# Kernel optimization log

Hardware: AMD Instinct MI355X
Metric: run time of the kernel (lower is better)

Reference implementation:

```python
import jax, jax.numpy as jnp
import numpy as np

N_NODES = 50000
N_EDGES = 800000
IN_DIM = 256
HIDDEN = 32
HEADS = 4
OUT_DIM = 64


def setup_inputs() -> dict:
    key = jax.random.key(0)
    k1, k2, k3, k4, k5, k6, k7 = jax.random.split(key, 7)
    h = jax.random.normal(k1, (N_NODES, IN_DIM), dtype=jnp.float32)
    src = jax.random.randint(k2, (N_EDGES,), 0, N_NODES, dtype=jnp.int32)
    dst = jax.random.randint(k3, (N_EDGES,), 0, N_NODES, dtype=jnp.int32)
    # xavier_normal with relu gain, per-head weights
    gain = float(np.sqrt(2.0))
    W1 = gain * jnp.sqrt(2.0 / (IN_DIM + HIDDEN)) * jax.random.normal(k4, (HEADS, IN_DIM, HIDDEN), dtype=jnp.float32)
    a1 = gain * jnp.sqrt(2.0 / (2 * HIDDEN + 1)) * jax.random.normal(k5, (HEADS, 2 * HIDDEN), dtype=jnp.float32)
    W2 = gain * jnp.sqrt(2.0 / (HIDDEN * HEADS + OUT_DIM)) * jax.random.normal(k6, (1, HIDDEN * HEADS, OUT_DIM), dtype=jnp.float32)
    a2 = gain * jnp.sqrt(2.0 / (2 * OUT_DIM + 1)) * jax.random.normal(k7, (1, 2 * OUT_DIM), dtype=jnp.float32)
    return {"h": h, "src": src, "dst": dst, "W1": W1, "a1": a1, "W2": W2, "a2": a2}


def _gat_layer(x, src, dst, W, a):
    # x: [N, in], W: [H, in, d], a: [H, 2d]
    N = x.shape[0]
    d = W.shape[-1]
    z = jnp.einsum('ni,hio->nho', x, W)                    # [N, H, d]
    a_s, a_d = a[:, :d], a[:, d:]
    es = jnp.einsum('nho,ho->nh', z, a_s)                  # per-node src score
    ed = jnp.einsum('nho,ho->nh', z, a_d)                  # per-node dst score
    e = jax.nn.leaky_relu(es[src] + ed[dst])               # [E, H]
    # segment (per-destination) softmax over incoming edges
    emax = jax.ops.segment_max(e, dst, num_segments=N)     # [N, H]
    ex = jnp.exp(e - emax[dst])
    denom = jax.ops.segment_sum(ex, dst, num_segments=N)   # [N, H]
    alpha = ex / denom[dst]                                # [E, H]
    # scatter weighted sum of source feats back to destinations
    out = jax.ops.segment_sum(alpha[:, :, None] * z[src], dst, num_segments=N)  # [N, H, d]
    return out.reshape(N, -1)


def reference(h, src, dst, W1, a1, W2, a2):
    h1 = jax.nn.elu(_gat_layer(h, src, dst, W1, a1))       # [N, HEADS*HIDDEN]
    return _gat_layer(h1, src, dst, W2, a2)                # [N, OUT_DIM]
```

## Files before the change

### kernel.cpp

```cpp
#include <hip/hip_runtime.h>
#include <hip/hip_bf16.h>
#include <math.h>

#define N_NODES 50000
#define N_EDGES 800000
#define IN_DIM 256
#define HID 32
#define HEADS 4
#define OUT_DIM 64

#define SCAN_CHUNK 1024
#define SCAN_BLOCKS ((N_NODES + SCAN_CHUNK - 1) / SCAN_CHUNK)
#define HIST_BLOCKS ((N_EDGES + 255) / 256)
#define MBLK ((N_NODES + 63) / 64)

typedef __attribute__((ext_vector_type(8))) short bf16x8;
typedef __attribute__((ext_vector_type(4))) float f32x4;

__device__ __forceinline__ float lrelu(float e) { return e > 0.f ? e : 0.01f * e; }
__device__ __forceinline__ float bflo(unsigned u) { return __uint_as_float(u << 16); }
__device__ __forceinline__ float bfhi(unsigned u) { return __uint_as_float(u & 0xffff0000u); }

__device__ __forceinline__ unsigned short rne_bf16(float x) {
    unsigned u = __float_as_uint(x);
    unsigned r = u + 0x7fffu + ((u >> 16) & 1u);
    return (unsigned short)(r >> 16);
}

__device__ __forceinline__ void splitf(float x, short& hi, short& lo) {
    unsigned u = __float_as_uint(x);
    unsigned short h = (unsigned short)(u >> 16);
    float hf = __uint_as_float(((unsigned)h) << 16);
    float l = x - hf;
    unsigned short lb = (unsigned short)(__float_as_uint(l) >> 16);
    hi = (short)h;
    lo = (short)lb;
}


__device__ __forceinline__ void prep_body(int k, int c,
        const float* __restrict__ W1, const float* __restrict__ a1,
        const float* __restrict__ W2, const float* __restrict__ a2,
        unsigned short* __restrict__ B1h, unsigned short* __restrict__ B1l,
        unsigned short* __restrict__ B2h, unsigned short* __restrict__ B2l) {
    if (c < 144) {
        float val = 0.f;
        if (c < 128) {
            val = W1[(size_t)(c >> 5) * IN_DIM * HID + (size_t)k * HID + (c & 31)];
        } else if (c < 136) {
            int j = c - 128;
            int hd = (j < 4) ? j : (j - 4);
            int off = (j < 4) ? 0 : HID;
            const float* Wp = W1 + (size_t)hd * IN_DIM * HID + (size_t)k * HID;
            const float* ap = a1 + hd * 2 * HID + off;
            float s = 0.f;
            for (int o = 0; o < HID; o++) s += Wp[o] * ap[o];
            val = s;
        }
        unsigned short hi = rne_bf16(val);
        float hf = __uint_as_float(((unsigned)hi) << 16);
        unsigned short lo = rne_bf16(val - hf);
        int s_ = k >> 5, q = (k >> 3) & 3, j8 = k & 7;
        int nt = c >> 4, L = q * 16 + (c & 15);
        size_t idx = (((size_t)s_ * 9 + nt) * 64 + L) * 8 + j8;
        B1h[idx] = hi;
        B1l[idx] = lo;
    } else if (c >= 160 && c < 240 && k < 128) {
        int c2 = c - 160;
        float val = 0.f;
        if (c2 < 64) {
            val = W2[(size_t)k * OUT_DIM + c2];
        } else if (c2 < 66) {
            const float* ap = a2 + (c2 - 64) * OUT_DIM;
            const float* Wp = W2 + (size_t)k * OUT_DIM;
            float s = 0.f;
            for (int o = 0; o < OUT_DIM; o++) s += Wp[o] * ap[o];
            val = s;
        }
        unsigned short hi = rne_bf16(val);
        float hf = __uint_as_float(((unsigned)hi) << 16);
        unsigned short lo = rne_bf16(val - hf);
        int s_ = k >> 5, q = (k >> 3) & 3, j8 = k & 7;
        int nt = c2 >> 4, L = q * 16 + (c2 & 15);
        size_t idx = (((size_t)s_ * 5 + nt) * 64 + L) * 8 + j8;
        B2h[idx] = hi;
        B2l[idx] = lo;
    }
}


__global__ void __launch_bounds__(256) prep_hist_kernel(
        const float* __restrict__ W1, const float* __restrict__ a1,
        const float* __restrict__ W2, const float* __restrict__ a2,
        unsigned short* __restrict__ B1h, unsigned short* __restrict__ B1l,
        unsigned short* __restrict__ B2h, unsigned short* __restrict__ B2l,
        const int* __restrict__ dst, int* __restrict__ count,
        int* __restrict__ rank) {
    int bid = blockIdx.x;
    if (bid < 256) {
        prep_body(bid, threadIdx.x, W1, a1, W2, a2, B1h, B1l, B2h, B2l);
    } else {
        int i = (bid - 256) * 256 + threadIdx.x;
        if (i < N_EDGES) rank[i] = atomicAdd(&count[dst[i]], 1);
    }
}


__device__ __forceinline__ void scan1_body(int bid, int t, const int* __restrict__ count,
        int* __restrict__ rs_local, int* __restrict__ bs_prefix, int* sdata) {
    int base = bid * SCAN_CHUNK + t * 4;
    int v[4];
    int s = 0;
#pragma unroll
    for (int j = 0; j < 4; j++) {
        int idx = base + j;
        int x = (idx < N_NODES) ? count[idx] : 0;
        v[j] = x;
        s += x;
    }
    sdata[t] = s;
    __syncthreads();
    for (int off = 1; off < 256; off <<= 1) {
        int u = (t >= off) ? sdata[t - off] : 0;
        __syncthreads();
        sdata[t] += u;
        __syncthreads();
    }
    int excl = sdata[t] - s;
#pragma unroll
    for (int j = 0; j < 4; j++) {
        int idx = base + j;
        if (idx < N_NODES) rs_local[idx] = excl;
        excl += v[j];
    }
    if (t > bid && t < SCAN_BLOCKS) atomicAdd(&bs_prefix[t], sdata[255]);
}


__device__ __forceinline__ void proj1_body(int n0, int L,
        const float* __restrict__ h, const unsigned short* __restrict__ Bh,
        const unsigned short* __restrict__ Bl, __hip_bfloat16* __restrict__ z1b,
        float* __restrict__ es1, float* __restrict__ ed1) {
    int q = L >> 4, L15 = L & 15;
    int rowA = n0 + L15;
    int rrA = rowA < N_NODES ? rowA : N_NODES - 1;
    const float* hrow = h + (size_t)rrA * IN_DIM + q * 8;

    f32x4 acc[9];
#pragma unroll
    for (int nt = 0; nt < 9; nt++) acc[nt] = (f32x4)(0.f);

    float4 x0 = *(const float4*)(hrow);
    float4 x1 = *(const float4*)(hrow + 4);

#pragma unroll
    for (int s = 0; s < 8; s++) {
        int sn = (s < 7) ? s + 1 : 7;
        float4 p0 = *(const float4*)(hrow + sn * 32);
        float4 p1 = *(const float4*)(hrow + sn * 32 + 4);

        float xs[8] = {x0.x, x0.y, x0.z, x0.w, x1.x, x1.y, x1.z, x1.w};
        bf16x8 ah, al;
#pragma unroll
        for (int j = 0; j < 8; j++) {
            short hi, lo;
            splitf(xs[j], hi, lo);
            ah[j] = hi;
            al[j] = lo;
        }

        const bf16x8* bhp = (const bf16x8*)(Bh + ((size_t)s * 9 * 64) * 8 + (size_t)L * 8);
        const bf16x8* blp = (const bf16x8*)(Bl + ((size_t)s * 9 * 64) * 8 + (size_t)L * 8);
#pragma unroll
        for (int nt = 0; nt < 9; nt++) {
            bf16x8 bh = bhp[nt * 64];
            acc[nt] = __builtin_amdgcn_mfma_f32_16x16x32_bf16(ah, bh, acc[nt], 0, 0, 0);
            acc[nt] = __builtin_amdgcn_mfma_f32_16x16x32_bf16(al, bh, acc[nt], 0, 0, 0);
        }
        {
            bf16x8 bl8 = blp[8 * 64];
            acc[8] = __builtin_amdgcn_mfma_f32_16x16x32_bf16(ah, bl8, acc[8], 0, 0, 0);
        }
        x0 = p0;
        x1 = p1;
    }

#pragma unroll
    for (int r = 0; r < 4; r++) {
        int rowc = n0 + q * 4 + r;
        if (rowc < N_NODES) {
#pragma unroll
            for (int nt = 0; nt < 8; nt++)
                z1b[(size_t)rowc * 128 + nt * 16 + L15] = __float2bfloat16(acc[nt][r]);
            if (L15 < 4) es1[rowc * HEADS + L15] = acc[8][r];
            else if (L15 < 8) ed1[rowc * HEADS + (L15 - 4)] = acc[8][r];
        }
    }
}


__global__ void __launch_bounds__(256) scan_proj1_kernel(
        const float* __restrict__ h, const unsigned short* __restrict__ Bh,
        const unsigned short* __restrict__ Bl, __hip_bfloat16* __restrict__ z1b,
        float* __restrict__ es1, float* __restrict__ ed1,
        const int* __restrict__ count, int* __restrict__ rs_local,
        int* __restrict__ bs_prefix) {
    if (blockIdx.x < SCAN_BLOCKS) {
        __shared__ int sdata[256];
        scan1_body(blockIdx.x, threadIdx.x, count, rs_local, bs_prefix, sdata);
        return;
    }
    int wave = threadIdx.x >> 6;
    int L = threadIdx.x & 63;
    int n0 = (blockIdx.x - SCAN_BLOCKS) * 64 + wave * 16;
    proj1_body(n0, L, h, Bh, Bl, z1b, es1, ed1);
}


__global__ void scatter_kernel(const int* __restrict__ src, const int* __restrict__ dst,
                               const int* __restrict__ rank, const int* __restrict__ rs_local,
                               const int* __restrict__ bs_prefix, int* __restrict__ esrc) {
    int i = blockIdx.x * blockDim.x + threadIdx.x;
    if (i < N_EDGES) {
        int d = dst[i];
        esrc[rs_local[d] + bs_prefix[d >> 10] + rank[i]] = src[i];
    }
}


__global__ void __launch_bounds__(256) agg1_kernel(
        const __hip_bfloat16* __restrict__ z1b, const float* __restrict__ es1,
        const float* __restrict__ ed1, const int* __restrict__ rs_local,
        const int* __restrict__ bs_prefix, const int* __restrict__ count,
        const int* __restrict__ esrc, __hip_bfloat16* __restrict__ h1b) {
    int v = blockIdx.x * 4 + (threadIdx.x >> 6);
    int L = threadIdx.x & 63;
    int sub = L >> 4;
    int c16 = L & 15;
    int hd = c16 >> 2;
    int beg = rs_local[v] + bs_prefix[v >> 10], deg = count[v];
    float edv = ed1[v * HEADS + hd];
    const int* ep = esrc + beg;
    float lacc = 0.f;
    float acc[8];
#pragma unroll
    for (int i = 0; i < 8; i++) acc[i] = 0.f;
    const uint4* zq = (const uint4*)z1b;

    for (int j0 = 0; j0 < deg; j0 += 32) {
        int se[8];
        uint4 u[8];
        float ev[8];
#pragma unroll
        for (int g = 0; g < 8; g++) {
            if (j0 + g * 4 < deg) {
                int e = j0 + g * 4 + sub;
                se[g] = ep[(e < deg) ? e : 0];
            }
        }
#pragma unroll
        for (int g = 0; g < 8; g++) {
            if (j0 + g * 4 < deg) {
                u[g] = zq[(size_t)se[g] * 16 + c16];
                ev[g] = es1[se[g] * HEADS + hd];
            }
        }
#pragma unroll
        for (int g = 0; g < 8; g++) {
            if (j0 + g * 4 < deg) {
                bool val = (j0 + g * 4 + sub) < deg;
                float q = val ? __expf(lrelu(ev[g] + edv)) : 0.f;
                lacc += q;
                acc[0] = fmaf(q, bflo(u[g].x), acc[0]);
                acc[1] = fmaf(q, bfhi(u[g].x), acc[1]);
                acc[2] = fmaf(q, bflo(u[g].y), acc[2]);
                acc[3] = fmaf(q, bfhi(u[g].y), acc[3]);
                acc[4] = fmaf(q, bflo(u[g].z), acc[4]);
                acc[5] = fmaf(q, bfhi(u[g].z), acc[5]);
                acc[6] = fmaf(q, bflo(u[g].w), acc[6]);
                acc[7] = fmaf(q, bfhi(u[g].w), acc[7]);
            }
        }
    }
    lacc += __shfl_xor(lacc, 1);
    lacc += __shfl_xor(lacc, 2);
    lacc += __shfl_xor(lacc, 16);
    lacc += __shfl_xor(lacc, 32);
    lacc *= 0.25f;
#pragma unroll
    for (int i = 0; i < 8; i++) {
        acc[i] += __shfl_xor(acc[i], 16);
        acc[i] += __shfl_xor(acc[i], 32);
    }
    if (L < 16) {
        float inv = (deg > 0) ? 1.f / lacc : 0.f;
        unsigned w[4];
#pragma unroll
        for (int i = 0; i < 4; i++) {
            float r0 = acc[2 * i] * inv;
            float r1 = acc[2 * i + 1] * inv;
            r0 = r0 > 0.f ? r0 : __expf(r0) - 1.f;
            r1 = r1 > 0.f ? r1 : __expf(r1) - 1.f;
            w[i] = (unsigned)rne_bf16(r0) | ((unsigned)rne_bf16(r1) << 16);
        }
        uint4* dstp = (uint4*)(h1b + (size_t)v * 128 + c16 * 8);
        *dstp = make_uint4(w[0], w[1], w[2], w[3]);
    }
}


__global__ void __launch_bounds__(256) proj2_mfma(
        const __hip_bfloat16* __restrict__ h1b, const unsigned short* __restrict__ Bh,
        const unsigned short* __restrict__ Bl, __hip_bfloat16* __restrict__ z2b,
        float* __restrict__ es2, float* __restrict__ ed2) {
    int tid = threadIdx.x;
    int wave = tid >> 6;
    int L = tid & 63;
    int q = L >> 4, L15 = L & 15;
    int n0 = blockIdx.x * 64 + wave * 16;

    int rowA = n0 + L15;
    int rrA = rowA < N_NODES ? rowA : N_NODES - 1;
    const bf16x8* hq = (const bf16x8*)(h1b + (size_t)rrA * 128);

    f32x4 acc[5];
#pragma unroll
    for (int nt = 0; nt < 5; nt++) acc[nt] = (f32x4)(0.f);

#pragma unroll
    for (int s = 0; s < 4; s++) {
        bf16x8 a = hq[s * 4 + q];
        const bf16x8* bhp = (const bf16x8*)(Bh + ((size_t)s * 5 * 64) * 8 + (size_t)L * 8);
        const bf16x8* blp = (const bf16x8*)(Bl + ((size_t)s * 5 * 64) * 8 + (size_t)L * 8);
#pragma unroll
        for (int nt = 0; nt < 5; nt++)
            acc[nt] = __builtin_amdgcn_mfma_f32_16x16x32_bf16(a, bhp[nt * 64], acc[nt], 0, 0, 0);
        acc[4] = __builtin_amdgcn_mfma_f32_16x16x32_bf16(a, blp[4 * 64], acc[4], 0, 0, 0);
    }

#pragma unroll
    for (int r = 0; r < 4; r++) {
        int rowc = n0 + q * 4 + r;
        if (rowc < N_NODES) {
#pragma unroll
            for (int nt = 0; nt < 4; nt++)
                z2b[(size_t)rowc * OUT_DIM + nt * 16 + L15] = __float2bfloat16(acc[nt][r]);
            if (L15 == 0) es2[rowc] = acc[4][r];
            else if (L15 == 1) ed2[rowc] = acc[4][r];
        }
    }
}


__global__ void __launch_bounds__(256) agg2_kernel(
        const __hip_bfloat16* __restrict__ z2b, const float* __restrict__ es2,
        const float* __restrict__ ed2, const int* __restrict__ rs_local,
        const int* __restrict__ bs_prefix, const int* __restrict__ count,
        const int* __restrict__ esrc, float* __restrict__ out) {
    int v = blockIdx.x * 4 + (threadIdx.x >> 6);
    int L = threadIdx.x & 63;
    int sub = L >> 3;
    int c8 = L & 7;
    int beg = rs_local[v] + bs_prefix[v >> 10], deg = count[v];
    float edv = ed2[v];
    const int* ep = esrc + beg;
    float lacc = 0.f;
    float acc[8];
#pragma unroll
    for (int i = 0; i < 8; i++) acc[i] = 0.f;
    const uint4* zq = (const uint4*)z2b;

    for (int j0 = 0; j0 < deg; j0 += 32) {
        int se[4];
        uint4 u[4];
        float ev[4];
#pragma unroll
        for (int g = 0; g < 4; g++) {
            if (j0 + g * 8 < deg) {
                int e = j0 + g * 8 + sub;
                se[g] = ep[(e < deg) ? e : 0];
            }
        }
#pragma unroll
        for (int g = 0; g < 4; g++) {
            if (j0 + g * 8 < deg) {
                u[g] = zq[(size_t)se[g] * 8 + c8];
                ev[g] = es2[se[g]];
            }
        }
#pragma unroll
        for (int g = 0; g < 4; g++) {
            if (j0 + g * 8 < deg) {
                bool val = (j0 + g * 8 + sub) < deg;
                float q = val ? __expf(lrelu(ev[g] + edv)) : 0.f;
                lacc += q;
                acc[0] = fmaf(q, bflo(u[g].x), acc[0]);
                acc[1] = fmaf(q, bfhi(u[g].x), acc[1]);
                acc[2] = fmaf(q, bflo(u[g].y), acc[2]);
                acc[3] = fmaf(q, bfhi(u[g].y), acc[3]);
                acc[4] = fmaf(q, bflo(u[g].z), acc[4]);
                acc[5] = fmaf(q, bfhi(u[g].z), acc[5]);
                acc[6] = fmaf(q, bflo(u[g].w), acc[6]);
                acc[7] = fmaf(q, bfhi(u[g].w), acc[7]);
            }
        }
    }
    lacc += __shfl_xor(lacc, 8);
    lacc += __shfl_xor(lacc, 16);
    lacc += __shfl_xor(lacc, 32);
#pragma unroll
    for (int i = 0; i < 8; i++) {
        acc[i] += __shfl_xor(acc[i], 8);
        acc[i] += __shfl_xor(acc[i], 16);
        acc[i] += __shfl_xor(acc[i], 32);
    }
    if (L < 8) {
        float inv = (deg > 0) ? 1.f / lacc : 0.f;
        float4 r0, r1;
#pragma unroll
        for (int i = 0; i < 8; i++) {
            float r = acc[i] * inv;
            if (i < 4) (&r0.x)[i] = r;
            else (&r1.x)[i - 4] = r;
        }
        float* dstp = out + (size_t)v * OUT_DIM + c8 * 8;
        *(float4*)dstp = r0;
        *(float4*)(dstp + 4) = r1;
    }
}


extern "C" void kernel_launch(void* const* d_in, const int* in_sizes, int n_in,
                              void* d_out, int out_size, void* d_ws, size_t ws_size,
                              hipStream_t stream) {
    const float* h  = (const float*)d_in[0];
    const int* src  = (const int*)d_in[1];
    const int* dst  = (const int*)d_in[2];
    const float* W1 = (const float*)d_in[3];
    const float* a1 = (const float*)d_in[4];
    const float* W2 = (const float*)d_in[5];
    const float* a2 = (const float*)d_in[6];
    float* out = (float*)d_out;

    char* w = (char*)d_ws;
    size_t off = 0;
    auto alloc = [&](size_t bytes) {
        void* p = w + off;
        off = (off + bytes + 255) & ~(size_t)255;
        return p;
    };
    __hip_bfloat16* z1b = (__hip_bfloat16*)alloc((size_t)N_NODES * 128 * 2);
    float* es1 = (float*)alloc((size_t)N_NODES * HEADS * 4);
    float* ed1 = (float*)alloc((size_t)N_NODES * HEADS * 4);
    __hip_bfloat16* h1b = (__hip_bfloat16*)alloc((size_t)N_NODES * 128 * 2);
    __hip_bfloat16* z2b = (__hip_bfloat16*)alloc((size_t)N_NODES * OUT_DIM * 2);
    float* es2 = (float*)alloc((size_t)N_NODES * 4);
    float* ed2 = (float*)alloc((size_t)N_NODES * 4);
    int* count     = (int*)alloc((size_t)(N_NODES + 64) * 4);
    int* bs_prefix = count + N_NODES;
    int* rs_local  = (int*)alloc((size_t)N_NODES * 4);
    int* rank      = (int*)alloc((size_t)N_EDGES * 4);
    int* esrc      = (int*)alloc((size_t)N_EDGES * 4);
    unsigned short* Bf1h = (unsigned short*)alloc((size_t)8 * 9 * 64 * 8 * 2);
    unsigned short* Bf1l = (unsigned short*)alloc((size_t)8 * 9 * 64 * 8 * 2);
    unsigned short* Bf2h = (unsigned short*)alloc((size_t)4 * 5 * 64 * 8 * 2);
    unsigned short* Bf2l = (unsigned short*)alloc((size_t)4 * 5 * 64 * 8 * 2);

    hipMemsetAsync(count, 0, (size_t)(N_NODES + 64) * 4, stream);

    prep_hist_kernel<<<256 + HIST_BLOCKS, 256, 0, stream>>>(
        W1, a1, W2, a2, Bf1h, Bf1l, Bf2h, Bf2l, dst, count, rank);

    scan_proj1_kernel<<<SCAN_BLOCKS + MBLK, 256, 0, stream>>>(
        h, Bf1h, Bf1l, z1b, es1, ed1, count, rs_local, bs_prefix);

    scatter_kernel<<<HIST_BLOCKS, 256, 0, stream>>>(src, dst, rank, rs_local, bs_prefix, esrc);

    agg1_kernel<<<N_NODES / 4, 256, 0, stream>>>(z1b, es1, ed1, rs_local, bs_prefix, count, esrc, h1b);
    proj2_mfma<<<MBLK, 256, 0, stream>>>(h1b, Bf2h, Bf2l, z2b, es2, ed2);
    agg2_kernel<<<N_NODES / 4, 256, 0, stream>>>(z2b, es2, ed2, rs_local, bs_prefix, count, esrc, out);
}
```

Before: 225.9 us.

## Rebalance kernel partitions to co-schedule proj1 with histogram and agg1 with proj2

Moves the degree histogram into the same launch as the first 500 proj1 tiles, and moves the scan into the launch with the remaining proj1 tiles. Splits agg1 at a node boundary so the second half of aggregation shares a launch with the proj2 tiles for the first half, followed by a small proj2 tail kernel. The memset is replaced by zeroing count inside the prep kernel. The aim is to fill idle CUs and cut launch gaps by overlapping independent work, at the cost of one extra launch and careful dependency ordering across the split ranges.

```diff
diff --git a/kernel.cpp b/kernel.cpp
--- a/kernel.cpp
+++ b/kernel.cpp
@@ -13,6 +13,15 @@
 #define SCAN_BLOCKS ((N_NODES + SCAN_CHUNK - 1) / SCAN_CHUNK)
 #define HIST_BLOCKS ((N_EDGES + 255) / 256)
 #define MBLK ((N_NODES + 63) / 64)
+
+#define PS1 500
+#define PS2 (MBLK - PS1)
+
+#define AGG_SPLIT 25024
+#define AGG1A_BLKS (AGG_SPLIT / 4)
+#define AGG1B_BLKS ((N_NODES - AGG_SPLIT + 3) / 4)
+#define P2A_BLKS (AGG_SPLIT / 64)
+#define P2B_BLKS ((N_NODES - AGG_SPLIT + 63) / 64)
 
 typedef __attribute__((ext_vector_type(8))) short bf16x8;
 typedef __attribute__((ext_vector_type(4))) float f32x4;
@@ -89,51 +98,15 @@
 }
 
 
-__global__ void __launch_bounds__(256) prep_hist_kernel(
+__global__ void __launch_bounds__(256) prep_kernel(
         const float* __restrict__ W1, const float* __restrict__ a1,
         const float* __restrict__ W2, const float* __restrict__ a2,
         unsigned short* __restrict__ B1h, unsigned short* __restrict__ B1l,
         unsigned short* __restrict__ B2h, unsigned short* __restrict__ B2l,
-        const int* __restrict__ dst, int* __restrict__ count,
-        int* __restrict__ rank) {
-    int bid = blockIdx.x;
-    if (bid < 256) {
-        prep_body(bid, threadIdx.x, W1, a1, W2, a2, B1h, B1l, B2h, B2l);
-    } else {
-        int i = (bid - 256) * 256 + threadIdx.x;
-        if (i < N_EDGES) rank[i] = atomicAdd(&count[dst[i]], 1);
-    }
-}
-
-
-__device__ __forceinline__ void scan1_body(int bid, int t, const int* __restrict__ count,
-        int* __restrict__ rs_local, int* __restrict__ bs_prefix, int* sdata) {
-    int base = bid * SCAN_CHUNK + t * 4;
-    int v[4];
-    int s = 0;
-#pragma unroll
-    for (int j = 0; j < 4; j++) {
-        int idx = base + j;
-        int x = (idx < N_NODES) ? count[idx] : 0;
-        v[j] = x;
-        s += x;
-    }
-    sdata[t] = s;
-    __syncthreads();
-    for (int off = 1; off < 256; off <<= 1) {
-        int u = (t >= off) ? sdata[t - off] : 0;
-        __syncthreads();
-        sdata[t] += u;
-        __syncthreads();
-    }
-    int excl = sdata[t] - s;
-#pragma unroll
-    for (int j = 0; j < 4; j++) {
-        int idx = base + j;
-        if (idx < N_NODES) rs_local[idx] = excl;
-        excl += v[j];
-    }
-    if (t > bid && t < SCAN_BLOCKS) atomicAdd(&bs_prefix[t], sdata[255]);
+        int* __restrict__ count) {
+    int gid = blockIdx.x * 256 + threadIdx.x;
+    if (gid < N_NODES + 64) count[gid] = 0;
+    prep_body(blockIdx.x, threadIdx.x, W1, a1, W2, a2, B1h, B1l, B2h, B2l);
 }
 
 
@@ -199,7 +172,56 @@
 }
 
 
-__global__ void __launch_bounds__(256) scan_proj1_kernel(
+__global__ void __launch_bounds__(256) proj1_hist_kernel(
+        const float* __restrict__ h, const unsigned short* __restrict__ Bh,
+        const unsigned short* __restrict__ Bl, __hip_bfloat16* __restrict__ z1b,
+        float* __restrict__ es1, float* __restrict__ ed1,
+        const int* __restrict__ dst, int* __restrict__ count,
+        int* __restrict__ rank) {
+    int bid = blockIdx.x;
+    if (bid < PS1) {
+        int wave = threadIdx.x >> 6;
+        int L = threadIdx.x & 63;
+        proj1_body(bid * 64 + wave * 16, L, h, Bh, Bl, z1b, es1, ed1);
+    } else {
+        int i = (bid - PS1) * 256 + threadIdx.x;
+        if (i < N_EDGES) rank[i] = atomicAdd(&count[dst[i]], 1);
+    }
+}
+
+
+__device__ __forceinline__ void scan1_body(int bid, int t, const int* __restrict__ count,
+        int* __restrict__ rs_local, int* __restrict__ bs_prefix, int* sdata) {
+    int base = bid * SCAN_CHUNK + t * 4;
+    int v[4];
+    int s = 0;
+#pragma unroll
+    for (int j = 0; j < 4; j++) {
+        int idx = base + j;
+        int x = (idx < N_NODES) ? count[idx] : 0;
+        v[j] = x;
+        s += x;
+    }
+    sdata[t] = s;
+    __syncthreads();
+    for (int off = 1; off < 256; off <<= 1) {
+        int u = (t >= off) ? sdata[t - off] : 0;
+        __syncthreads();
+        sdata[t] += u;
+        __syncthreads();
+    }
+    int excl = sdata[t] - s;
+#pragma unroll
+    for (int j = 0; j < 4; j++) {
+        int idx = base + j;
+        if (idx < N_NODES) rs_local[idx] = excl;
+        excl += v[j];
+    }
+    if (t > bid && t < SCAN_BLOCKS) atomicAdd(&bs_prefix[t], sdata[255]);
+}
+
+
+__global__ void __launch_bounds__(256) scan_proj1b_kernel(
         const float* __restrict__ h, const unsigned short* __restrict__ Bh,
         const unsigned short* __restrict__ Bl, __hip_bfloat16* __restrict__ z1b,
         float* __restrict__ es1, float* __restrict__ ed1,
@@ -210,10 +232,10 @@
         scan1_body(blockIdx.x, threadIdx.x, count, rs_local, bs_prefix, sdata);
         return;
     }
+    int task = blockIdx.x - SCAN_BLOCKS + PS1;
     int wave = threadIdx.x >> 6;
     int L = threadIdx.x & 63;
-    int n0 = (blockIdx.x - SCAN_BLOCKS) * 64 + wave * 16;
-    proj1_body(n0, L, h, Bh, Bl, z1b, es1, ed1);
+    proj1_body(task * 64 + wave * 16, L, h, Bh, Bl, z1b, es1, ed1);
 }
 
 
@@ -228,13 +250,11 @@
 }
 
 
-__global__ void __launch_bounds__(256) agg1_kernel(
+__device__ __forceinline__ void agg1_body(int v, int L,
         const __hip_bfloat16* __restrict__ z1b, const float* __restrict__ es1,
         const float* __restrict__ ed1, const int* __restrict__ rs_local,
         const int* __restrict__ bs_prefix, const int* __restrict__ count,
         const int* __restrict__ esrc, __hip_bfloat16* __restrict__ h1b) {
-    int v = blockIdx.x * 4 + (threadIdx.x >> 6);
-    int L = threadIdx.x & 63;
     int sub = L >> 4;
     int c16 = L & 15;
     int hd = c16 >> 2;
@@ -309,16 +329,11 @@
 }
 
 
-__global__ void __launch_bounds__(256) proj2_mfma(
+__device__ __forceinline__ void proj2_body(int n0, int L,
         const __hip_bfloat16* __restrict__ h1b, const unsigned short* __restrict__ Bh,
         const unsigned short* __restrict__ Bl, __hip_bfloat16* __restrict__ z2b,
         float* __restrict__ es2, float* __restrict__ ed2) {
-    int tid = threadIdx.x;
-    int wave = tid >> 6;
-    int L = tid & 63;
     int q = L >> 4, L15 = L & 15;
-    int n0 = blockIdx.x * 64 + wave * 16;
-
     int rowA = n0 + L15;
     int rrA = rowA < N_NODES ? rowA : N_NODES - 1;
     const bf16x8* hq = (const bf16x8*)(h1b + (size_t)rrA * 128);
@@ -349,6 +364,46 @@
             else if (L15 == 1) ed2[rowc] = acc[4][r];
         }
     }
+}
+
+
+__global__ void __launch_bounds__(256) agg1a_kernel(
+        const __hip_bfloat16* __restrict__ z1b, const float* __restrict__ es1,
+        const float* __restrict__ ed1, const int* __restrict__ rs_local,
+        const int* __restrict__ bs_prefix, const int* __restrict__ count,
+        const int* __restrict__ esrc, __hip_bfloat16* __restrict__ h1b) {
+    int v = blockIdx.x * 4 + (threadIdx.x >> 6);
+    agg1_body(v, threadIdx.x & 63, z1b, es1, ed1, rs_local, bs_prefix, count, esrc, h1b);
+}
+
+
+__global__ void __launch_bounds__(256) agg1b_proj2a_kernel(
+        const __hip_bfloat16* __restrict__ z1b, const float* __restrict__ es1,
+        const float* __restrict__ ed1, const int* __restrict__ rs_local,
+        const int* __restrict__ bs_prefix, const int* __restrict__ count,
+        const int* __restrict__ esrc, __hip_bfloat16* __restrict__ h1b,
+        const unsigned short* __restrict__ B2h, const unsigned short* __restrict__ B2l,
+        __hip_bfloat16* __restrict__ z2b, float* __restrict__ es2,
+        float* __restrict__ ed2) {
+    int L = threadIdx.x & 63;
+    int wave = threadIdx.x >> 6;
+    if (blockIdx.x < AGG1B_BLKS) {
+        int v = AGG_SPLIT + blockIdx.x * 4 + wave;
+        agg1_body(v, L, z1b, es1, ed1, rs_local, bs_prefix, count, esrc, h1b);
+    } else {
+        int pb = blockIdx.x - AGG1B_BLKS;
+        proj2_body(pb * 64 + wave * 16, L, h1b, B2h, B2l, z2b, es2, ed2);
+    }
+}
+
+
+__global__ void __launch_bounds__(256) proj2b_kernel(
+        const __hip_bfloat16* __restrict__ h1b, const unsigned short* __restrict__ Bh,
+        const unsigned short* __restrict__ Bl, __hip_bfloat16* __restrict__ z2b,
+        float* __restrict__ es2, float* __restrict__ ed2) {
+    int wave = threadIdx.x >> 6;
+    int L = threadIdx.x & 63;
+    proj2_body(AGG_SPLIT + blockIdx.x * 64 + wave * 16, L, h1b, Bh, Bl, z2b, es2, ed2);
 }
 
 
@@ -466,17 +521,25 @@
     unsigned short* Bf2h = (unsigned short*)alloc((size_t)4 * 5 * 64 * 8 * 2);
     unsigned short* Bf2l = (unsigned short*)alloc((size_t)4 * 5 * 64 * 8 * 2);
 
-    hipMemsetAsync(count, 0, (size_t)(N_NODES + 64) * 4, stream);
-
-    prep_hist_kernel<<<256 + HIST_BLOCKS, 256, 0, stream>>>(
-        W1, a1, W2, a2, Bf1h, Bf1l, Bf2h, Bf2l, dst, count, rank);
-
-    scan_proj1_kernel<<<SCAN_BLOCKS + MBLK, 256, 0, stream>>>(
+    prep_kernel<<<256, 256, 0, stream>>>(W1, a1, W2, a2, Bf1h, Bf1l, Bf2h, Bf2l, count);
+
+    proj1_hist_kernel<<<PS1 + HIST_BLOCKS, 256, 0, stream>>>(
+        h, Bf1h, Bf1l, z1b, es1, ed1, dst, count, rank);
+
+    scan_proj1b_kernel<<<SCAN_BLOCKS + PS2, 256, 0, stream>>>(
         h, Bf1h, Bf1l, z1b, es1, ed1, count, rs_local, bs_prefix);
 
     scatter_kernel<<<HIST_BLOCKS, 256, 0, stream>>>(src, dst, rank, rs_local, bs_prefix, esrc);
 
-    agg1_kernel<<<N_NODES / 4, 256, 0, stream>>>(z1b, es1, ed1, rs_local, bs_prefix, count, esrc, h1b);
-    proj2_mfma<<<MBLK, 256, 0, stream>>>(h1b, Bf2h, Bf2l, z2b, es2, ed2);
-    agg2_kernel<<<N_NODES / 4, 256, 0, stream>>>(z2b, es2, ed2, rs_local, bs_prefix, count, esrc, out);
-}
+    agg1a_kernel<<<AGG1A_BLKS, 256, 0, stream>>>(
+        z1b, es1, ed1, rs_local, bs_prefix, count, esrc, h1b);
+
+    agg1b_proj2a_kernel<<<AGG1B_BLKS + P2A_BLKS, 256, 0, stream>>>(
+        z1b, es1, ed1, rs_local, bs_prefix, count, esrc, h1b,
+        Bf2h, Bf2l, z2b, es2, ed2);
+
+    proj2b_kernel<<<P2B_BLKS, 256, 0, stream>>>(h1b, Bf2h, Bf2l, z2b, es2, ed2);
+
+    agg2_kernel<<<N_NODES / 4, 256, 0, stream>>>(
+        z2b, es2, ed2, rs_local, bs_prefix, count, esrc, out);
+}
```

Measured after the change: 232.9 us. +3.1%, slower.

## Split layer-1 projection across scan and scatter launches; preload A operands

Applied to the files above, without the earlier changes.

The layer-1 projection blocks are split into two parts: the first part runs alongside the prefix-scan blocks and the rest runs alongside the edge-scatter blocks, replacing the separate scatter launch. This fills the otherwise short scatter kernel with MFMA work and balances the two launches. The projection and proj2 kernels also load all A-operand rows up front instead of software-prefetching them one step ahead, which raises register pressure. The split point is a fixed constant.

```diff
diff --git a/kernel.cpp b/kernel.cpp
--- a/kernel.cpp
+++ b/kernel.cpp
@@ -13,6 +13,9 @@
 #define SCAN_BLOCKS ((N_NODES + SCAN_CHUNK - 1) / SCAN_CHUNK)
 #define HIST_BLOCKS ((N_EDGES + 255) / 256)
 #define MBLK ((N_NODES + 63) / 64)
+
+#define PS1 500
+#define PS2 (MBLK - PS1)
 
 typedef __attribute__((ext_vector_type(8))) short bf16x8;
 typedef __attribute__((ext_vector_type(4))) float f32x4;
@@ -146,20 +149,21 @@
     int rrA = rowA < N_NODES ? rowA : N_NODES - 1;
     const float* hrow = h + (size_t)rrA * IN_DIM + q * 8;
 
+    float4 xv0[8], xv1[8];
+#pragma unroll
+    for (int s = 0; s < 8; s++) {
+        xv0[s] = *(const float4*)(hrow + s * 32);
+        xv1[s] = *(const float4*)(hrow + s * 32 + 4);
+    }
+
     f32x4 acc[9];
 #pragma unroll
     for (int nt = 0; nt < 9; nt++) acc[nt] = (f32x4)(0.f);
 
-    float4 x0 = *(const float4*)(hrow);
-    float4 x1 = *(const float4*)(hrow + 4);
-
 #pragma unroll
     for (int s = 0; s < 8; s++) {
-        int sn = (s < 7) ? s + 1 : 7;
-        float4 p0 = *(const float4*)(hrow + sn * 32);
-        float4 p1 = *(const float4*)(hrow + sn * 32 + 4);
-
-        float xs[8] = {x0.x, x0.y, x0.z, x0.w, x1.x, x1.y, x1.z, x1.w};
+        float xs[8] = {xv0[s].x, xv0[s].y, xv0[s].z, xv0[s].w,
+                       xv1[s].x, xv1[s].y, xv1[s].z, xv1[s].w};
         bf16x8 ah, al;
 #pragma unroll
         for (int j = 0; j < 8; j++) {
@@ -181,8 +185,6 @@
             bf16x8 bl8 = blp[8 * 64];
             acc[8] = __builtin_amdgcn_mfma_f32_16x16x32_bf16(ah, bl8, acc[8], 0, 0, 0);
         }
-        x0 = p0;
-        x1 = p1;
     }
 
 #pragma unroll
@@ -199,28 +201,37 @@
 }
 
 
-__global__ void __launch_bounds__(256) scan_proj1_kernel(
+__global__ void __launch_bounds__(256) proj1a_scan_kernel(
         const float* __restrict__ h, const unsigned short* __restrict__ Bh,
         const unsigned short* __restrict__ Bl, __hip_bfloat16* __restrict__ z1b,
         float* __restrict__ es1, float* __restrict__ ed1,
         const int* __restrict__ count, int* __restrict__ rs_local,
         int* __restrict__ bs_prefix) {
-    if (blockIdx.x < SCAN_BLOCKS) {
-        __shared__ int sdata[256];
-        scan1_body(blockIdx.x, threadIdx.x, count, rs_local, bs_prefix, sdata);
+    if (blockIdx.x < PS1) {
+        int wave = threadIdx.x >> 6;
+        int L = threadIdx.x & 63;
+        proj1_body(blockIdx.x * 64 + wave * 16, L, h, Bh, Bl, z1b, es1, ed1);
         return;
     }
-    int wave = threadIdx.x >> 6;
-    int L = threadIdx.x & 63;
-    int n0 = (blockIdx.x - SCAN_BLOCKS) * 64 + wave * 16;
-    proj1_body(n0, L, h, Bh, Bl, z1b, es1, ed1);
-}
-
-
-__global__ void scatter_kernel(const int* __restrict__ src, const int* __restrict__ dst,
-                               const int* __restrict__ rank, const int* __restrict__ rs_local,
-                               const int* __restrict__ bs_prefix, int* __restrict__ esrc) {
-    int i = blockIdx.x * blockDim.x + threadIdx.x;
+    __shared__ int sdata[256];
+    scan1_body(blockIdx.x - PS1, threadIdx.x, count, rs_local, bs_prefix, sdata);
+}
+
+
+__global__ void __launch_bounds__(256) proj1b_scatter_kernel(
+        const float* __restrict__ h, const unsigned short* __restrict__ Bh,
+        const unsigned short* __restrict__ Bl, __hip_bfloat16* __restrict__ z1b,
+        float* __restrict__ es1, float* __restrict__ ed1,
+        const int* __restrict__ src, const int* __restrict__ dst,
+        const int* __restrict__ rank, const int* __restrict__ rs_local,
+        const int* __restrict__ bs_prefix, int* __restrict__ esrc) {
+    if (blockIdx.x < PS2) {
+        int wave = threadIdx.x >> 6;
+        int L = threadIdx.x & 63;
+        proj1_body((blockIdx.x + PS1) * 64 + wave * 16, L, h, Bh, Bl, z1b, es1, ed1);
+        return;
+    }
+    int i = (blockIdx.x - PS2) * 256 + threadIdx.x;
     if (i < N_EDGES) {
         int d = dst[i];
         esrc[rs_local[d] + bs_prefix[d >> 10] + rank[i]] = src[i];
@@ -323,19 +334,22 @@
     int rrA = rowA < N_NODES ? rowA : N_NODES - 1;
     const bf16x8* hq = (const bf16x8*)(h1b + (size_t)rrA * 128);
 
+    bf16x8 av[4];
+#pragma unroll
+    for (int s = 0; s < 4; s++) av[s] = hq[s * 4 + q];
+
     f32x4 acc[5];
 #pragma unroll
     for (int nt = 0; nt < 5; nt++) acc[nt] = (f32x4)(0.f);
 
 #pragma unroll
     for (int s = 0; s < 4; s++) {
-        bf16x8 a = hq[s * 4 + q];
         const bf16x8* bhp = (const bf16x8*)(Bh + ((size_t)s * 5 * 64) * 8 + (size_t)L * 8);
         const bf16x8* blp = (const bf16x8*)(Bl + ((size_t)s * 5 * 64) * 8 + (size_t)L * 8);
 #pragma unroll
         for (int nt = 0; nt < 5; nt++)
-            acc[nt] = __builtin_amdgcn_mfma_f32_16x16x32_bf16(a, bhp[nt * 64], acc[nt], 0, 0, 0);
-        acc[4] = __builtin_amdgcn_mfma_f32_16x16x32_bf16(a, blp[4 * 64], acc[4], 0, 0, 0);
+            acc[nt] = __builtin_amdgcn_mfma_f32_16x16x32_bf16(av[s], bhp[nt * 64], acc[nt], 0, 0, 0);
+        acc[4] = __builtin_amdgcn_mfma_f32_16x16x32_bf16(av[s], blp[4 * 64], acc[4], 0, 0, 0);
     }
 
 #pragma unroll
@@ -471,12 +485,15 @@
     prep_hist_kernel<<<256 + HIST_BLOCKS, 256, 0, stream>>>(
         W1, a1, W2, a2, Bf1h, Bf1l, Bf2h, Bf2l, dst, count, rank);
 
-    scan_proj1_kernel<<<SCAN_BLOCKS + MBLK, 256, 0, stream>>>(
+    proj1a_scan_kernel<<<PS1 + SCAN_BLOCKS, 256, 0, stream>>>(
         h, Bf1h, Bf1l, z1b, es1, ed1, count, rs_local, bs_prefix);
 
-    scatter_kernel<<<HIST_BLOCKS, 256, 0, stream>>>(src, dst, rank, rs_local, bs_prefix, esrc);
-
-    agg1_kernel<<<N_NODES / 4, 256, 0, stream>>>(z1b, es1, ed1, rs_local, bs_prefix, count, esrc, h1b);
+    proj1b_scatter_kernel<<<PS2 + HIST_BLOCKS, 256, 0, stream>>>(
+        h, Bf1h, Bf1l, z1b, es1, ed1, src, dst, rank, rs_local, bs_prefix, esrc);
+
+    agg1_kernel<<<N_NODES / 4, 256, 0, stream>>>(
+        z1b, es1, ed1, rs_local, bs_prefix, count, esrc, h1b);
     proj2_mfma<<<MBLK, 256, 0, stream>>>(h1b, Bf2h, Bf2l, z2b, es2, ed2);
-    agg2_kernel<<<N_NODES / 4, 256, 0, stream>>>(z2b, es2, ed2, rs_local, bs_prefix, count, esrc, out);
-}
+    agg2_kernel<<<N_NODES / 4, 256, 0, stream>>>(
+        z2b, es2, ed2, rs_local, bs_prefix, count, esrc, out);
+}
```

Result: slower. 234.5 us (+3.8%).

## Replace per-edge rank array with cursor atomics and pack z1 stores in pairs

Applied to the files above, without the earlier changes.

The histogram pass no longer stores a per-edge rank. The scan initialises a per-node cursor, and the scatter kernel claims slots with an atomicAdd on that cursor, which removes the rank write and read traffic. The layer-1 projection now writes z1 as packed bf16 pairs. The W2 rows are permuted in prep to match the new column order of h1. proj2 also hoists its A-operand loads ahead of the MFMA loop. The cost is atomic contention in the scatter kernel and a non-deterministic edge order within each destination segment, which can change the summation order.

```diff
diff --git a/kernel.cpp b/kernel.cpp
--- a/kernel.cpp
+++ b/kernel.cpp
@@ -67,12 +67,13 @@
         B1l[idx] = lo;
     } else if (c >= 160 && c < 240 && k < 128) {
         int c2 = c - 160;
+        int ck = (2 * (k >> 5) + (k & 1)) * 16 + ((k & 31) >> 1);
         float val = 0.f;
         if (c2 < 64) {
-            val = W2[(size_t)k * OUT_DIM + c2];
+            val = W2[(size_t)ck * OUT_DIM + c2];
         } else if (c2 < 66) {
             const float* ap = a2 + (c2 - 64) * OUT_DIM;
-            const float* Wp = W2 + (size_t)k * OUT_DIM;
+            const float* Wp = W2 + (size_t)ck * OUT_DIM;
             float s = 0.f;
             for (int o = 0; o < OUT_DIM; o++) s += Wp[o] * ap[o];
             val = s;
@@ -94,20 +95,20 @@
         const float* __restrict__ W2, const float* __restrict__ a2,
         unsigned short* __restrict__ B1h, unsigned short* __restrict__ B1l,
         unsigned short* __restrict__ B2h, unsigned short* __restrict__ B2l,
-        const int* __restrict__ dst, int* __restrict__ count,
-        int* __restrict__ rank) {
+        const int* __restrict__ dst, int* __restrict__ count) {
     int bid = blockIdx.x;
     if (bid < 256) {
         prep_body(bid, threadIdx.x, W1, a1, W2, a2, B1h, B1l, B2h, B2l);
     } else {
         int i = (bid - 256) * 256 + threadIdx.x;
-        if (i < N_EDGES) rank[i] = atomicAdd(&count[dst[i]], 1);
+        if (i < N_EDGES) atomicAdd(&count[dst[i]], 1);
     }
 }
 
 
 __device__ __forceinline__ void scan1_body(int bid, int t, const int* __restrict__ count,
-        int* __restrict__ rs_local, int* __restrict__ bs_prefix, int* sdata) {
+        int* __restrict__ rs_local, int* __restrict__ cursor,
+        int* __restrict__ bs_prefix, int* sdata) {
     int base = bid * SCAN_CHUNK + t * 4;
     int v[4];
     int s = 0;
@@ -130,7 +131,10 @@
 #pragma unroll
     for (int j = 0; j < 4; j++) {
         int idx = base + j;
-        if (idx < N_NODES) rs_local[idx] = excl;
+        if (idx < N_NODES) {
+            rs_local[idx] = excl;
+            cursor[idx] = excl;
+        }
         excl += v[j];
     }
     if (t > bid && t < SCAN_BLOCKS) atomicAdd(&bs_prefix[t], sdata[255]);
@@ -189,9 +193,13 @@
     for (int r = 0; r < 4; r++) {
         int rowc = n0 + q * 4 + r;
         if (rowc < N_NODES) {
-#pragma unroll
-            for (int nt = 0; nt < 8; nt++)
-                z1b[(size_t)rowc * 128 + nt * 16 + L15] = __float2bfloat16(acc[nt][r]);
+            unsigned* zp = (unsigned*)(z1b + (size_t)rowc * 128);
+#pragma unroll
+            for (int hh = 0; hh < 4; hh++) {
+                unsigned wv = (unsigned)rne_bf16(acc[2 * hh][r]) |
+                              ((unsigned)rne_bf16(acc[2 * hh + 1][r]) << 16);
+                zp[hh * 16 + L15] = wv;
+            }
             if (L15 < 4) es1[rowc * HEADS + L15] = acc[8][r];
             else if (L15 < 8) ed1[rowc * HEADS + (L15 - 4)] = acc[8][r];
         }
@@ -204,10 +212,10 @@
         const unsigned short* __restrict__ Bl, __hip_bfloat16* __restrict__ z1b,
         float* __restrict__ es1, float* __restrict__ ed1,
         const int* __restrict__ count, int* __restrict__ rs_local,
-        int* __restrict__ bs_prefix) {
+        int* __restrict__ cursor, int* __restrict__ bs_prefix) {
     if (blockIdx.x < SCAN_BLOCKS) {
         __shared__ int sdata[256];
-        scan1_body(blockIdx.x, threadIdx.x, count, rs_local, bs_prefix, sdata);
+        scan1_body(blockIdx.x, threadIdx.x, count, rs_local, cursor, bs_prefix, sdata);
         return;
     }
     int wave = threadIdx.x >> 6;
@@ -218,12 +226,13 @@
 
 
 __global__ void scatter_kernel(const int* __restrict__ src, const int* __restrict__ dst,
-                               const int* __restrict__ rank, const int* __restrict__ rs_local,
-                               const int* __restrict__ bs_prefix, int* __restrict__ esrc) {
+                               int* __restrict__ cursor, const int* __restrict__ bs_prefix,
+                               int* __restrict__ esrc) {
     int i = blockIdx.x * blockDim.x + threadIdx.x;
     if (i < N_EDGES) {
         int d = dst[i];
-        esrc[rs_local[d] + bs_prefix[d >> 10] + rank[i]] = src[i];
+        int pos = atomicAdd(&cursor[d], 1);
+        esrc[pos + bs_prefix[d >> 10]] = src[i];
     }
 }
 
@@ -323,19 +332,22 @@
     int rrA = rowA < N_NODES ? rowA : N_NODES - 1;
     const bf16x8* hq = (const bf16x8*)(h1b + (size_t)rrA * 128);
 
+    bf16x8 av[4];
+#pragma unroll
+    for (int s = 0; s < 4; s++) av[s] = hq[s * 4 + q];
+
     f32x4 acc[5];
 #pragma unroll
     for (int nt = 0; nt < 5; nt++) acc[nt] = (f32x4)(0.f);
 
 #pragma unroll
     for (int s = 0; s < 4; s++) {
-        bf16x8 a = hq[s * 4 + q];
         const bf16x8* bhp = (const bf16x8*)(Bh + ((size_t)s * 5 * 64) * 8 + (size_t)L * 8);
         const bf16x8* blp = (const bf16x8*)(Bl + ((size_t)s * 5 * 64) * 8 + (size_t)L * 8);
 #pragma unroll
         for (int nt = 0; nt < 5; nt++)
-            acc[nt] = __builtin_amdgcn_mfma_f32_16x16x32_bf16(a, bhp[nt * 64], acc[nt], 0, 0, 0);
-        acc[4] = __builtin_amdgcn_mfma_f32_16x16x32_bf16(a, blp[4 * 64], acc[4], 0, 0, 0);
+            acc[nt] = __builtin_amdgcn_mfma_f32_16x16x32_bf16(av[s], bhp[nt * 64], acc[nt], 0, 0, 0);
+        acc[4] = __builtin_amdgcn_mfma_f32_16x16x32_bf16(av[s], blp[4 * 64], acc[4], 0, 0, 0);
     }
 
 #pragma unroll
@@ -459,7 +471,7 @@
     int* count     = (int*)alloc((size_t)(N_NODES + 64) * 4);
     int* bs_prefix = count + N_NODES;
     int* rs_local  = (int*)alloc((size_t)N_NODES * 4);
-    int* rank      = (int*)alloc((size_t)N_EDGES * 4);
+    int* cursor    = (int*)alloc((size_t)N_NODES * 4);
     int* esrc      = (int*)alloc((size_t)N_EDGES * 4);
     unsigned short* Bf1h = (unsigned short*)alloc((size_t)8 * 9 * 64 * 8 * 2);
     unsigned short* Bf1l = (unsigned short*)alloc((size_t)8 * 9 * 64 * 8 * 2);
@@ -469,14 +481,16 @@
     hipMemsetAsync(count, 0, (size_t)(N_NODES + 64) * 4, stream);
 
     prep_hist_kernel<<<256 + HIST_BLOCKS, 256, 0, stream>>>(
-        W1, a1, W2, a2, Bf1h, Bf1l, Bf2h, Bf2l, dst, count, rank);
+        W1, a1, W2, a2, Bf1h, Bf1l, Bf2h, Bf2l, dst, count);
 
     scan_proj1_kernel<<<SCAN_BLOCKS + MBLK, 256, 0, stream>>>(
-        h, Bf1h, Bf1l, z1b, es1, ed1, count, rs_local, bs_prefix);
-
-    scatter_kernel<<<HIST_BLOCKS, 256, 0, stream>>>(src, dst, rank, rs_local, bs_prefix, esrc);
-
-    agg1_kernel<<<N_NODES / 4, 256, 0, stream>>>(z1b, es1, ed1, rs_local, bs_prefix, count, esrc, h1b);
+        h, Bf1h, Bf1l, z1b, es1, ed1, count, rs_local, cursor, bs_prefix);
+
+    scatter_kernel<<<HIST_BLOCKS, 256, 0, stream>>>(src, dst, cursor, bs_prefix, esrc);
+
+    agg1_kernel<<<N_NODES / 4, 256, 0, stream>>>(
+        z1b, es1, ed1, rs_local, bs_prefix, count, esrc, h1b);
     proj2_mfma<<<MBLK, 256, 0, stream>>>(h1b, Bf2h, Bf2l, z2b, es2, ed2);
-    agg2_kernel<<<N_NODES / 4, 256, 0, stream>>>(z2b, es2, ed2, rs_local, bs_prefix, count, esrc, out);
-}
+    agg2_kernel<<<N_NODES / 4, 256, 0, stream>>>(
+        z2b, es2, ed2, rs_local, bs_prefix, count, esrc, out);
+}
```

After: 264.0 us. 16.9% more time.
